# Kernel tuning notes

Measured on AMD Instinct MI355X. Metric: run time of the kernel, lower is better.

The kernel has to match this reference:

```python
import jax, jax.numpy as jnp
import numpy as np

N_INST, BATCH, IN_DIM, L_DIM = 256, 128, 1024, 512

def setup_inputs() -> dict:
    key = jax.random.key(0)
    k1, k2, k3, k4 = jax.random.split(key, 4)
    # glorot-uniform-ish scales
    sv = np.sqrt(6.0 / (IN_DIM + L_DIM)).astype(np.float32)
    sw = np.sqrt(6.0 / (L_DIM + 1)).astype(np.float32)
    x = jax.random.normal(k1, (N_INST, BATCH, IN_DIM), dtype=jnp.float32)
    v = jax.random.uniform(k2, (IN_DIM, L_DIM), minval=-sv, maxval=sv, dtype=jnp.float32)
    u = jax.random.uniform(k3, (IN_DIM, L_DIM), minval=-sv, maxval=sv, dtype=jnp.float32)
    w = jax.random.uniform(k4, (L_DIM, 1), minval=-sw, maxval=sw, dtype=jnp.float32)
    return {"x": x, "v": v, "u": u, "w": w}

def reference(x, v, u, w):
    # x: [n_instances, batch, in_dim]
    # Fused batched version of the per-instance loop:
    # score_i = (tanh(x_i @ v) * sigmoid(x_i @ u)) @ w, softmax over instances.
    h = jnp.tanh(jnp.einsum('nbd,dl->nbl', x, v))          # [n, b, l]
    g = jax.nn.sigmoid(jnp.einsum('nbd,dl->nbl', x, u))    # [n, b, l]
    scores = jnp.einsum('nbl,lo->nbo', h * g, w)            # [n, b, 1]
    alpha = jax.nn.softmax(scores, axis=0)                  # softmax over instance axis
    return alpha
```

## Files before the change

### kernel.cpp

```cpp
#include <hip/hip_runtime.h>
#include <stdint.h>

typedef unsigned int  u32;
typedef unsigned short u16;
typedef __bf16 v8bf __attribute__((ext_vector_type(8)));
typedef float  v4f  __attribute__((ext_vector_type(4)));

#define N_INST 256
#define BATCH  128
#define IN_DIM 1024
#define L_DIM  512
#define M_TOT  (N_INST*BATCH)

#define BM 128
#define BN 128
#define BK 64
#define KITERS (IN_DIM/BK)

#define XB_BYTES   ((size_t)M_TOT * IN_DIM * 2)
#define WPK_BYTES  ((size_t)1024 * IN_DIM * 2)

__device__ inline u32 f2bf_pk(float a, float b){
  u32 ua = __builtin_bit_cast(u32, a);
  u32 ub = __builtin_bit_cast(u32, b);
  ua = (ua + 0x7FFFu + ((ua >> 16) & 1u)) >> 16;
  ub = (ub + 0x7FFFu + ((ub >> 16) & 1u)) & 0xFFFF0000u;
  return ua | ub;
}

__device__ inline void gl2lds16(const u16* g, u16* l){
  __builtin_amdgcn_global_load_lds(
      (const __attribute__((address_space(1))) u32*)(g),
      (__attribute__((address_space(3))) u32*)(l), 16, 0, 0);
}

#define PREP_XBLKS 16384
__global__ void prep(const float* __restrict__ x, const float* __restrict__ v,
                     const float* __restrict__ u, u16* __restrict__ xb,
                     u16* __restrict__ wpk){
  const int b = blockIdx.x;
  if (b < PREP_XBLKS){
    size_t o = ((size_t)b * 256 + threadIdx.x) * 8;
    float4 a0 = *reinterpret_cast<const float4*>(x + o);
    float4 a1 = *reinterpret_cast<const float4*>(x + o + 4);
    uint4 out;
    out.x = f2bf_pk(a0.x, a0.y); out.y = f2bf_pk(a0.z, a0.w);
    out.z = f2bf_pk(a1.x, a1.y); out.w = f2bf_pk(a1.z, a1.w);
    *reinterpret_cast<uint4*>(xb + o) = out;
  } else {
    int t = (b - PREP_XBLKS) * 256 + threadIdx.x;
    int o = t * 8;
    int np = o >> 10;
    int k0 = o & 1023;
    int l  = np >> 1;
    const float* src = (np & 1) ? u : v;
    u32 out[4];
#pragma unroll
    for (int i = 0; i < 4; ++i){
      float a = src[(size_t)(k0 + 2*i    ) * L_DIM + l];
      float c = src[(size_t)(k0 + 2*i + 1) * L_DIM + l];
      out[i] = f2bf_pk(a, c);
    }
    *reinterpret_cast<uint4*>(wpk + o) = make_uint4(out[0], out[1], out[2], out[3]);
  }
}

__launch_bounds__(256)
__global__ void gemm_score(const u16* __restrict__ xb, const u16* __restrict__ wpk,
                           const float* __restrict__ w, float* __restrict__ partial){
  __shared__ __align__(16) u16 As[BM * BK];
  __shared__ __align__(16) u16 Bs[BN * BK];
  __shared__ float ssum[BM];

  const int tid  = threadIdx.x;
  const u32 bid  = blockIdx.x;
  const int xcd  = bid & 7;
  const int slot = bid >> 3;
  const int nblk = slot & 7;
  const int mblk = xcd * 32 + (slot >> 3);
  const int m0   = mblk * BM;

  const int lane = tid & 63;
  const int wave = tid >> 6;
  const int wm   = (wave >> 1) * 64;
  const int wn   = (wave & 1) * 64;
  const int q    = lane >> 4;
  const int c    = lane & 15;

  if (tid < BM) ssum[tid] = 0.f;

  const int rr = lane >> 3;
  const int cg = (lane & 7) ^ rr;
  const u16* ga = xb  + (size_t)m0 * IN_DIM;
  const u16* gb = wpk + (size_t)(nblk * BN) * IN_DIM;

  v4f acc[4][4];
#pragma unroll
  for (int i = 0; i < 4; ++i)
#pragma unroll
    for (int j = 0; j < 4; ++j)
      acc[i][j] = (v4f){0.f, 0.f, 0.f, 0.f};

  for (int kt = 0; kt < KITERS; ++kt){
    const int kb = kt * BK;
#pragma unroll
    for (int j = 0; j < 4; ++j){
      const int reg = wave * 4 + j;
      const int row = reg * 8 + rr;
      gl2lds16(ga + (size_t)row * IN_DIM + kb + cg * 8, &As[reg * 512 + lane * 8]);
      gl2lds16(gb + (size_t)row * IN_DIM + kb + cg * 8, &Bs[reg * 512 + lane * 8]);
    }
    __syncthreads();
#pragma unroll
    for (int kk = 0; kk < 2; ++kk){
      v8bf af[4], bfr[4];
#pragma unroll
      for (int i = 0; i < 4; ++i){
        const int row = wm + i*16 + c;
        const int ch  = (kk*4 + q) ^ (row & 7);
        af[i] = *reinterpret_cast<const v8bf*>(&As[row*64 + ch*8]);
      }
#pragma unroll
      for (int j = 0; j < 4; ++j){
        const int row = wn + j*16 + c;
        const int ch  = (kk*4 + q) ^ (row & 7);
        bfr[j] = *reinterpret_cast<const v8bf*>(&Bs[row*64 + ch*8]);
      }
#pragma unroll
      for (int i = 0; i < 4; ++i)
#pragma unroll
        for (int j = 0; j < 4; ++j)
          acc[i][j] = __builtin_amdgcn_mfma_f32_16x16x32_bf16(af[i], bfr[j], acc[i][j], 0, 0, 0);
    }
    __syncthreads();
  }

  float wl[4];
#pragma unroll
  for (int j = 0; j < 4; ++j)
    wl[j] = w[nblk*64 + (wn >> 1) + j*8 + (c >> 1)];

  const int codd = c & 1;
#pragma unroll
  for (int i = 0; i < 4; ++i){
    float rs[4] = {0.f, 0.f, 0.f, 0.f};
#pragma unroll
    for (int j = 0; j < 4; ++j){
#pragma unroll
      for (int r = 0; r < 4; ++r){
        float val = acc[i][j][r];
        float y = codd ? val : 2.f*val;
        float s = 1.f / (1.f + __expf(-y));
        float t = codd ? s : (2.f*s - 1.f);
        float part = __shfl_xor(t, 1, 64);
        rs[r] += codd ? 0.f : (t * part * wl[j]);
      }
    }
#pragma unroll
    for (int r = 0; r < 4; ++r){
      float v2 = rs[r];
      v2 += __shfl_xor(v2, 1, 64);
      v2 += __shfl_xor(v2, 2, 64);
      v2 += __shfl_xor(v2, 4, 64);
      v2 += __shfl_xor(v2, 8, 64);
      if (c == 0) atomicAdd(&ssum[wm + i*16 + q*4 + r], v2);
    }
  }
  __syncthreads();
  if (tid < BM) partial[(size_t)nblk * M_TOT + m0 + tid] = ssum[tid];
}

__global__ void softmax_inst(const float* __restrict__ partial, float* __restrict__ out){
  __shared__ float red[N_INST];
  const int b = blockIdx.x;
  const int n = threadIdx.x;
  float s = 0.f;
#pragma unroll
  for (int i = 0; i < 8; ++i) s += partial[(size_t)i * M_TOT + n*BATCH + b];
  red[n] = s; __syncthreads();
  for (int st = N_INST/2; st > 0; st >>= 1){
    if (n < st) red[n] = fmaxf(red[n], red[n + st]);
    __syncthreads();
  }
  float mx = red[0]; __syncthreads();
  float e = __expf(s - mx);
  red[n] = e; __syncthreads();
  for (int st = N_INST/2; st > 0; st >>= 1){
    if (n < st) red[n] += red[n + st];
    __syncthreads();
  }
  out[n*BATCH + b] = e / red[0];
}

extern "C" void kernel_launch(void* const* d_in, const int* in_sizes, int n_in,
                              void* d_out, int out_size, void* d_ws, size_t ws_size,
                              hipStream_t stream) {
  const float* x = (const float*)d_in[0];
  const float* v = (const float*)d_in[1];
  const float* u = (const float*)d_in[2];
  const float* w = (const float*)d_in[3];
  u16*   xb      = (u16*)d_ws;
  u16*   wpk     = (u16*)((char*)d_ws + XB_BYTES);
  float* partial = (float*)((char*)d_ws + XB_BYTES + WPK_BYTES);
  float* out     = (float*)d_out;

  prep<<<dim3(PREP_XBLKS + 512), dim3(256), 0, stream>>>(x, v, u, xb, wpk);
  gemm_score<<<dim3(2048), dim3(256), 0, stream>>>(xb, wpk, w, partial);
  softmax_inst<<<dim3(BATCH), dim3(N_INST), 0, stream>>>(partial, out);
}
```

Before: 312.7 us.

## Double-buffer GEMM LDS tiles and fuse instance softmax into last-arriving blocks

Adds a two-stage LDS double buffer so the next K tile's global-to-LDS loads are issued before computing the current tile, dropping one barrier per iteration. Partial scores are now accumulated with global atomics into a zeroed score buffer, and a global arrival counter lets the last 128 blocks wait for all others and compute the per-batch softmax, removing the separate softmax launch. LDS use doubles and launch bounds request two blocks per CU. The spin-wait relies on all blocks being resident or scheduled in order, and atomic summation order makes results nondeterministic.

```diff
diff --git a/kernel.cpp b/kernel.cpp
--- a/kernel.cpp
+++ b/kernel.cpp
@@ -16,9 +16,11 @@
 #define BN 128
 #define BK 64
 #define KITERS (IN_DIM/BK)
+#define GRID   2048
 
 #define XB_BYTES   ((size_t)M_TOT * IN_DIM * 2)
 #define WPK_BYTES  ((size_t)1024 * IN_DIM * 2)
+#define SCORE_BYTES ((size_t)M_TOT * 4)
 
 __device__ inline u32 f2bf_pk(float a, float b){
   u32 ua = __builtin_bit_cast(u32, a);
@@ -37,7 +39,8 @@
 #define PREP_XBLKS 16384
 __global__ void prep(const float* __restrict__ x, const float* __restrict__ v,
                      const float* __restrict__ u, u16* __restrict__ xb,
-                     u16* __restrict__ wpk){
+                     u16* __restrict__ wpk, float* __restrict__ score,
+                     u32* __restrict__ counter){
   const int b = blockIdx.x;
   if (b < PREP_XBLKS){
     size_t o = ((size_t)b * 256 + threadIdx.x) * 8;
@@ -47,7 +50,7 @@
     out.x = f2bf_pk(a0.x, a0.y); out.y = f2bf_pk(a0.z, a0.w);
     out.z = f2bf_pk(a1.x, a1.y); out.w = f2bf_pk(a1.z, a1.w);
     *reinterpret_cast<uint4*>(xb + o) = out;
-  } else {
+  } else if (b < PREP_XBLKS + 512){
     int t = (b - PREP_XBLKS) * 256 + threadIdx.x;
     int o = t * 8;
     int np = o >> 10;
@@ -62,15 +65,24 @@
       out[i] = f2bf_pk(a, c);
     }
     *reinterpret_cast<uint4*>(wpk + o) = make_uint4(out[0], out[1], out[2], out[3]);
-  }
-}
-
-__launch_bounds__(256)
-__global__ void gemm_score(const u16* __restrict__ xb, const u16* __restrict__ wpk,
-                           const float* __restrict__ w, float* __restrict__ partial){
-  __shared__ __align__(16) u16 As[BM * BK];
-  __shared__ __align__(16) u16 Bs[BN * BK];
+  } else {
+    float4 z = {0.f,0.f,0.f,0.f};
+#pragma unroll
+    for (int i = 0; i < 32; ++i)
+      reinterpret_cast<float4*>(score)[threadIdx.x*32 + i] = z;
+    if (threadIdx.x == 0) *counter = 0u;
+  }
+}
+
+__launch_bounds__(256, 2)
+__global__ void gemm_fused(const u16* __restrict__ xb, const u16* __restrict__ wpk,
+                           const float* __restrict__ w, float* __restrict__ score,
+                           u32* counter, float* __restrict__ out){
+  __shared__ __align__(16) u16 As[2][BM * BK];
+  __shared__ __align__(16) u16 Bs[2][BN * BK];
   __shared__ float ssum[BM];
+  __shared__ float red[N_INST];
+  __shared__ u32 stick;
 
   const int tid  = threadIdx.x;
   const u32 bid  = blockIdx.x;
@@ -94,37 +106,49 @@
   const u16* ga = xb  + (size_t)m0 * IN_DIM;
   const u16* gb = wpk + (size_t)(nblk * BN) * IN_DIM;
 
-  v4f acc[4][4];
-#pragma unroll
-  for (int i = 0; i < 4; ++i)
-#pragma unroll
-    for (int j = 0; j < 4; ++j)
-      acc[i][j] = (v4f){0.f, 0.f, 0.f, 0.f};
-
-  for (int kt = 0; kt < KITERS; ++kt){
+  auto issue = [&](int kt, int pb){
     const int kb = kt * BK;
 #pragma unroll
     for (int j = 0; j < 4; ++j){
       const int reg = wave * 4 + j;
       const int row = reg * 8 + rr;
-      gl2lds16(ga + (size_t)row * IN_DIM + kb + cg * 8, &As[reg * 512 + lane * 8]);
-      gl2lds16(gb + (size_t)row * IN_DIM + kb + cg * 8, &Bs[reg * 512 + lane * 8]);
-    }
+      gl2lds16(ga + (size_t)row * IN_DIM + kb + cg * 8, &As[pb][reg * 512 + lane * 8]);
+      gl2lds16(gb + (size_t)row * IN_DIM + kb + cg * 8, &Bs[pb][reg * 512 + lane * 8]);
+    }
+  };
+
+  int aoff[2][4], boff[2][4];
+#pragma unroll
+  for (int kk = 0; kk < 2; ++kk)
+#pragma unroll
+    for (int i = 0; i < 4; ++i){
+      const int ra = wm + i*16 + c;
+      aoff[kk][i] = ra*64 + (((kk*4 + q) ^ (ra & 7)) * 8);
+      const int rb = wn + i*16 + c;
+      boff[kk][i] = rb*64 + (((kk*4 + q) ^ (rb & 7)) * 8);
+    }
+
+  v4f acc[4][4];
+#pragma unroll
+  for (int i = 0; i < 4; ++i)
+#pragma unroll
+    for (int j = 0; j < 4; ++j)
+      acc[i][j] = (v4f){0.f, 0.f, 0.f, 0.f};
+
+  issue(0, 0);
+  for (int kt = 0; kt < KITERS; ++kt){
+    const int pb = kt & 1;
     __syncthreads();
+    if (kt + 1 < KITERS) issue(kt + 1, pb ^ 1);
+    const u16* a = As[pb];
+    const u16* b = Bs[pb];
 #pragma unroll
     for (int kk = 0; kk < 2; ++kk){
       v8bf af[4], bfr[4];
 #pragma unroll
       for (int i = 0; i < 4; ++i){
-        const int row = wm + i*16 + c;
-        const int ch  = (kk*4 + q) ^ (row & 7);
-        af[i] = *reinterpret_cast<const v8bf*>(&As[row*64 + ch*8]);
-      }
-#pragma unroll
-      for (int j = 0; j < 4; ++j){
-        const int row = wn + j*16 + c;
-        const int ch  = (kk*4 + q) ^ (row & 7);
-        bfr[j] = *reinterpret_cast<const v8bf*>(&Bs[row*64 + ch*8]);
+        af[i]  = *reinterpret_cast<const v8bf*>(&a[aoff[kk][i]]);
+        bfr[i] = *reinterpret_cast<const v8bf*>(&b[boff[kk][i]]);
       }
 #pragma unroll
       for (int i = 0; i < 4; ++i)
@@ -132,7 +156,6 @@
         for (int j = 0; j < 4; ++j)
           acc[i][j] = __builtin_amdgcn_mfma_f32_16x16x32_bf16(af[i], bfr[j], acc[i][j], 0, 0, 0);
     }
-    __syncthreads();
   }
 
   float wl[4];
@@ -167,29 +190,39 @@
     }
   }
   __syncthreads();
-  if (tid < BM) partial[(size_t)nblk * M_TOT + m0 + tid] = ssum[tid];
-}
-
-__global__ void softmax_inst(const float* __restrict__ partial, float* __restrict__ out){
-  __shared__ float red[N_INST];
-  const int b = blockIdx.x;
-  const int n = threadIdx.x;
-  float s = 0.f;
-#pragma unroll
-  for (int i = 0; i < 8; ++i) s += partial[(size_t)i * M_TOT + n*BATCH + b];
-  red[n] = s; __syncthreads();
-  for (int st = N_INST/2; st > 0; st >>= 1){
-    if (n < st) red[n] = fmaxf(red[n], red[n + st]);
+  if (tid < BM) atomicAdd(&score[m0 + tid], ssum[tid]);
+  __threadfence();
+  __syncthreads();
+  if (tid == 0){
+    __threadfence();
+    stick = atomicAdd(counter, 1);
+  }
+  __syncthreads();
+  const u32 t = stick;
+
+  if (t >= (u32)(GRID - BATCH)){
+    const int b = (int)t - (GRID - BATCH);
+    if (tid == 0){
+      while (__hip_atomic_load(counter, __ATOMIC_RELAXED, __HIP_MEMORY_SCOPE_AGENT) < (u32)GRID)
+        __builtin_amdgcn_s_sleep(8);
+    }
     __syncthreads();
-  }
-  float mx = red[0]; __syncthreads();
-  float e = __expf(s - mx);
-  red[n] = e; __syncthreads();
-  for (int st = N_INST/2; st > 0; st >>= 1){
-    if (n < st) red[n] += red[n + st];
-    __syncthreads();
-  }
-  out[n*BATCH + b] = e / red[0];
+    __threadfence();
+    float s = __hip_atomic_load(&score[tid*BATCH + b], __ATOMIC_RELAXED, __HIP_MEMORY_SCOPE_AGENT);
+    red[tid] = s; __syncthreads();
+    for (int st = N_INST/2; st > 0; st >>= 1){
+      if (tid < st) red[tid] = fmaxf(red[tid], red[tid + st]);
+      __syncthreads();
+    }
+    float mx = red[0]; __syncthreads();
+    float e = __expf(s - mx);
+    red[tid] = e; __syncthreads();
+    for (int st = N_INST/2; st > 0; st >>= 1){
+      if (tid < st) red[tid] += red[tid + st];
+      __syncthreads();
+    }
+    out[tid*BATCH + b] = e / red[0];
+  }
 }
 
 extern "C" void kernel_launch(void* const* d_in, const int* in_sizes, int n_in,
@@ -201,10 +234,10 @@
   const float* w = (const float*)d_in[3];
   u16*   xb      = (u16*)d_ws;
   u16*   wpk     = (u16*)((char*)d_ws + XB_BYTES);
-  float* partial = (float*)((char*)d_ws + XB_BYTES + WPK_BYTES);
+  float* score   = (float*)((char*)d_ws + XB_BYTES + WPK_BYTES);
+  u32*   counter = (u32*)((char*)d_ws + XB_BYTES + WPK_BYTES + SCORE_BYTES);
   float* out     = (float*)d_out;
 
-  prep<<<dim3(PREP_XBLKS + 512), dim3(256), 0, stream>>>(x, v, u, xb, wpk);
-  gemm_score<<<dim3(2048), dim3(256), 0, stream>>>(xb, wpk, w, partial);
-  softmax_inst<<<dim3(BATCH), dim3(N_INST), 0, stream>>>(partial, out);
-}
+  prep<<<dim3(PREP_XBLKS + 512 + 1), dim3(256), 0, stream>>>(x, v, u, xb, wpk, score, counter);
+  gemm_fused<<<dim3(GRID), dim3(256), 0, stream>>>(xb, wpk, w, score, counter, out);
+}
```

Result: slower. 451.7 us (+44.5%).

## Repack V/U in 16-column groups to pair tanh/sigmoid per lane, drop LDS atomics

Applied to the files above, without the earlier changes.

The weight packing changes from interleaving V and U column by column to alternating groups of 16 columns. Each lane's accumulator tiles then hold matching tanh and sigmoid values, so the epilogue needs no shuffle to pair them and no odd/even lane masking. Each wave writes its own partial score slice directly, replacing the shared-memory atomics and block sync, and softmax now sums 16 slices instead of 8. The change also precomputes LDS fragment offsets and switches to a plain 2D grid, which drops the XCD-aware block remapping and may reduce L2 locality.

```diff
diff --git a/kernel.cpp b/kernel.cpp
--- a/kernel.cpp
+++ b/kernel.cpp
@@ -16,6 +16,7 @@
 #define BN 128
 #define BK 64
 #define KITERS (IN_DIM/BK)
+#define NSLICE 16
 
 #define XB_BYTES   ((size_t)M_TOT * IN_DIM * 2)
 #define WPK_BYTES  ((size_t)1024 * IN_DIM * 2)
@@ -52,8 +53,8 @@
     int o = t * 8;
     int np = o >> 10;
     int k0 = o & 1023;
-    int l  = np >> 1;
-    const float* src = (np & 1) ? u : v;
+    int l  = ((np >> 5) << 4) | (np & 15);
+    const float* src = ((np >> 4) & 1) ? u : v;
     u32 out[4];
 #pragma unroll
     for (int i = 0; i < 4; ++i){
@@ -70,14 +71,10 @@
                            const float* __restrict__ w, float* __restrict__ partial){
   __shared__ __align__(16) u16 As[BM * BK];
   __shared__ __align__(16) u16 Bs[BN * BK];
-  __shared__ float ssum[BM];
 
   const int tid  = threadIdx.x;
-  const u32 bid  = blockIdx.x;
-  const int xcd  = bid & 7;
-  const int slot = bid >> 3;
-  const int nblk = slot & 7;
-  const int mblk = xcd * 32 + (slot >> 3);
+  const int nblk = blockIdx.x;
+  const int mblk = blockIdx.y;
   const int m0   = mblk * BM;
 
   const int lane = tid & 63;
@@ -87,12 +84,19 @@
   const int q    = lane >> 4;
   const int c    = lane & 15;
 
-  if (tid < BM) ssum[tid] = 0.f;
-
   const int rr = lane >> 3;
   const int cg = (lane & 7) ^ rr;
   const u16* ga = xb  + (size_t)m0 * IN_DIM;
   const u16* gb = wpk + (size_t)(nblk * BN) * IN_DIM;
+
+  int aoff[4], boff[4];
+#pragma unroll
+  for (int i = 0; i < 4; ++i){
+    const int ra = wm + i*16 + c;
+    aoff[i] = ra*64 + ((q ^ (ra & 7)) * 8);
+    const int rb = wn + i*16 + c;
+    boff[i] = rb*64 + ((q ^ (rb & 7)) * 8);
+  }
 
   v4f acc[4][4];
 #pragma unroll
@@ -116,15 +120,8 @@
       v8bf af[4], bfr[4];
 #pragma unroll
       for (int i = 0; i < 4; ++i){
-        const int row = wm + i*16 + c;
-        const int ch  = (kk*4 + q) ^ (row & 7);
-        af[i] = *reinterpret_cast<const v8bf*>(&As[row*64 + ch*8]);
-      }
-#pragma unroll
-      for (int j = 0; j < 4; ++j){
-        const int row = wn + j*16 + c;
-        const int ch  = (kk*4 + q) ^ (row & 7);
-        bfr[j] = *reinterpret_cast<const v8bf*>(&Bs[row*64 + ch*8]);
+        af[i]  = *reinterpret_cast<const v8bf*>(&As[aoff[i] ^ (kk*32)]);
+        bfr[i] = *reinterpret_cast<const v8bf*>(&Bs[boff[i] ^ (kk*32)]);
       }
 #pragma unroll
       for (int i = 0; i < 4; ++i)
@@ -135,39 +132,28 @@
     __syncthreads();
   }
 
-  float wl[4];
-#pragma unroll
-  for (int j = 0; j < 4; ++j)
-    wl[j] = w[nblk*64 + (wn >> 1) + j*8 + (c >> 1)];
+  const int lbase = nblk*64 + (wn >> 5)*16 + c;
+  const float wl0 = w[lbase];
+  const float wl1 = w[lbase + 16];
+  const int p = nblk*2 + (wn >> 6);
+  float* pout = partial + (size_t)p * M_TOT + m0 + wm;
 
-  const int codd = c & 1;
 #pragma unroll
   for (int i = 0; i < 4; ++i){
-    float rs[4] = {0.f, 0.f, 0.f, 0.f};
-#pragma unroll
-    for (int j = 0; j < 4; ++j){
-#pragma unroll
-      for (int r = 0; r < 4; ++r){
-        float val = acc[i][j][r];
-        float y = codd ? val : 2.f*val;
-        float s = 1.f / (1.f + __expf(-y));
-        float t = codd ? s : (2.f*s - 1.f);
-        float part = __shfl_xor(t, 1, 64);
-        rs[r] += codd ? 0.f : (t * part * wl[j]);
-      }
-    }
 #pragma unroll
     for (int r = 0; r < 4; ++r){
-      float v2 = rs[r];
+      float t0 = 2.f / (1.f + __expf(-2.f * acc[i][0][r])) - 1.f;
+      float s0 = 1.f / (1.f + __expf(-acc[i][1][r]));
+      float t1 = 2.f / (1.f + __expf(-2.f * acc[i][2][r])) - 1.f;
+      float s1 = 1.f / (1.f + __expf(-acc[i][3][r]));
+      float v2 = t0*s0*wl0 + t1*s1*wl1;
       v2 += __shfl_xor(v2, 1, 64);
       v2 += __shfl_xor(v2, 2, 64);
       v2 += __shfl_xor(v2, 4, 64);
       v2 += __shfl_xor(v2, 8, 64);
-      if (c == 0) atomicAdd(&ssum[wm + i*16 + q*4 + r], v2);
+      if (c == 0) pout[i*16 + q*4 + r] = v2;
     }
   }
-  __syncthreads();
-  if (tid < BM) partial[(size_t)nblk * M_TOT + m0 + tid] = ssum[tid];
 }
 
 __global__ void softmax_inst(const float* __restrict__ partial, float* __restrict__ out){
@@ -176,7 +162,7 @@
   const int n = threadIdx.x;
   float s = 0.f;
 #pragma unroll
-  for (int i = 0; i < 8; ++i) s += partial[(size_t)i * M_TOT + n*BATCH + b];
+  for (int i = 0; i < NSLICE; ++i) s += partial[(size_t)i * M_TOT + n*BATCH + b];
   red[n] = s; __syncthreads();
   for (int st = N_INST/2; st > 0; st >>= 1){
     if (n < st) red[n] = fmaxf(red[n], red[n + st]);
@@ -205,6 +191,6 @@
   float* out     = (float*)d_out;
 
   prep<<<dim3(PREP_XBLKS + 512), dim3(256), 0, stream>>>(x, v, u, xb, wpk);
-  gemm_score<<<dim3(2048), dim3(256), 0, stream>>>(xb, wpk, w, partial);
+  gemm_score<<<dim3(8, 256), dim3(256), 0, stream>>>(xb, wpk, w, partial);
   softmax_inst<<<dim3(BATCH), dim3(N_INST), 0, stream>>>(partial, out);
 }
```

New measurement: 314.5 us. No clear change (+0.6%).
